# Kernel tuning notes

Measured on AMD Instinct MI355X. Metric: run time of the kernel, lower is better.

Reference implementation:

```python
import jax, jax.numpy as jnp
import numpy as np

B, S, D = 8, 1024, 1024
H = 2048            # expert hidden dim
E = 8               # num experts
TOP_K = 2
D_NOISE = 256
TEMP = 1.0


def setup_inputs() -> dict:
    key = jax.random.key(0)
    ks = jax.random.split(key, 8)
    return {
        "x": jax.random.normal(ks[0], (B, S, D), dtype=jnp.float32),
        "noise_clock_emb": jax.random.normal(ks[1], (B, D_NOISE), dtype=jnp.float32),
        # router weight [D_noise, E] (xavier-ish scale)
        "route_weight": jax.random.normal(ks[2], (D_NOISE, E), dtype=jnp.float32) * (1.0 / np.sqrt(D_NOISE)),
        # stacked expert params; torch Linear y = x @ W.T + b, stored here pre-transposed
        "fc_in_w": jax.random.normal(ks[3], (E, D, 2 * H), dtype=jnp.float32) * 0.02,
        "fc_in_b": jax.random.normal(ks[4], (E, 2 * H), dtype=jnp.float32) * 0.02,
        "fc_out_w": jax.random.normal(ks[5], (E, H, D), dtype=jnp.float32) * 0.02,
        "fc_out_b": jax.random.normal(ks[6], (E, D), dtype=jnp.float32) * 0.02,
    }


def reference(x, noise_clock_emb, route_weight, fc_in_w, fc_in_b, fc_out_w, fc_out_b):
    # ---- router: P = softmax(phi(sigma) @ W_R / T) ----
    logits = (noise_clock_emb @ route_weight) / TEMP            # [B, E]
    probs = jax.nn.softmax(logits, axis=-1)
    topk_weights, topk_indices = jax.lax.top_k(probs, TOP_K)    # [B, K]
    topk_weights = topk_weights / jnp.clip(
        topk_weights.sum(axis=-1, keepdims=True), 1e-8)
    # dense per-(batch, expert) mixing coefficient, identical to the
    # masked accumulation in the torch loop
    coeff = jnp.einsum("bke,bk->be",
                       jax.nn.one_hot(topk_indices, E, dtype=x.dtype),
                       topk_weights)                             # [B, E]

    # ---- all experts densely over the full batch (matches original math) ----
    h = jnp.einsum("bsd,edh->ebsh", x, fc_in_w) + fc_in_b[:, None, None, :]
    value, gate = jnp.split(h, 2, axis=-1)                       # [E,B,S,H] each
    hidden = value * jax.nn.silu(gate)
    mixed = jnp.einsum("ebsh,ehd,be->bsd", hidden, fc_out_w, coeff)
    mixed = mixed + jnp.einsum("be,ed->bd", coeff, fc_out_b)[:, None, :]
    return mixed, logits, probs, topk_indices, topk_weights
```

## Files before the change

### kernel.cpp

```cpp
#include <hip/hip_runtime.h>
#include <stdint.h>

#define B_ 8
#define S_ 1024
#define D_ 1024
#define H_ 2048
#define E_ 8
#define DN_ 256

typedef unsigned char u8;
typedef float f32x4 __attribute__((ext_vector_type(4)));
typedef long long ll;

__device__ __forceinline__ u8 f2f8(float f) {
  return (u8)(__builtin_amdgcn_cvt_pk_fp8_f32(f, f, 0, false) & 0xff);
}
__device__ __forceinline__ unsigned int pk4f8(float a, float b, float c, float d) {
  int w = __builtin_amdgcn_cvt_pk_fp8_f32(a, b, 0, false);
  w = __builtin_amdgcn_cvt_pk_fp8_f32(c, d, w, true);
  return (unsigned int)w;
}

__device__ __forceinline__ void gll16(const void* g, void* l) {
  __builtin_amdgcn_global_load_lds(
      (__attribute__((address_space(1))) void*)g,
      (__attribute__((address_space(3))) void*)l, 16, 0, 0);
}

__device__ __forceinline__ int swz(int r) { return (r & 3) ^ ((r >> 2) & 1); }

template <int R, int C>
__device__ __forceinline__ void transpose_body(const float* __restrict__ ip,
                                               u8* __restrict__ op,
                                               int bx, int by, int t,
                                               u8 (&tile)[64][72]) {
  const int r0 = by * 64, c0 = bx * 64;
  const int rr = t >> 4;
  const int c4 = t & 15;
#pragma unroll
  for (int i = 0; i < 4; ++i) {
    const int r = rr + i * 16;
    float4 v = *(const float4*)(ip + (size_t)(r0 + r) * C + c0 + c4 * 4);
    tile[c4 * 4 + 0][r] = f2f8(v.x);
    tile[c4 * 4 + 1][r] = f2f8(v.y);
    tile[c4 * 4 + 2][r] = f2f8(v.z);
    tile[c4 * 4 + 3][r] = f2f8(v.w);
  }
  __syncthreads();
#pragma unroll
  for (int i = 0; i < 4; ++i) {
    const int c = rr + i * 16;
    unsigned int w = *(const unsigned int*)&tile[c][c4 * 4];
    *(unsigned int*)(op + (size_t)(c0 + c) * R + r0 + c4 * 4) = w;
  }
}

#define NCAST (B_ * S_ * D_ / 1024)
#define NT1 ((2 * H_ / 64) * (D_ / 64) * E_)
#define NT2 ((D_ / 64) * (H_ / 64) * E_)

__global__ void __launch_bounds__(256) prep_kernel(
    const float* __restrict__ x, const float* __restrict__ noise,
    const float* __restrict__ rw, const float* __restrict__ fiw,
    const float* __restrict__ fow,
    float* __restrict__ out_logits, float* __restrict__ out_probs,
    float* __restrict__ out_idx, float* __restrict__ out_w,
    int* __restrict__ ws_idx, float* __restrict__ ws_w,
    unsigned int* __restrict__ xq, u8* __restrict__ wtin,
    u8* __restrict__ wtout) {
  __shared__ __align__(16) u8 tile[64][72];
  const int t = threadIdx.x;
  int bid = blockIdx.x;

  if (bid == 0) {
    float* sl = (float*)&tile[0][0];
    float* sp = sl + 64;
    {
      const int pair = t >> 2, sub = t & 3;
      const int b = pair >> 3, e = pair & 7;
      float acc = 0.f;
      const int d0 = sub * 64;
      for (int d = d0; d < d0 + 64; ++d)
        acc += noise[b * DN_ + d] * rw[d * E_ + e];
      acc += __shfl_xor(acc, 1);
      acc += __shfl_xor(acc, 2);
      if (sub == 0) sl[pair] = acc;
    }
    __syncthreads();
    if (t < 64) {
      const int b = t >> 3;
      float L = sl[t];
      out_logits[t] = L;
      float m = -1e30f;
      for (int j = 0; j < 8; ++j) m = fmaxf(m, sl[b * 8 + j]);
      float s = 0.f;
      for (int j = 0; j < 8; ++j) s += __expf(sl[b * 8 + j] - m);
      float p = __expf(L - m) / s;
      out_probs[t] = p;
      sp[t] = p;
    }
    __syncthreads();
    if (t < 64 && (t & 7) == 0) {
      const int b = t >> 3;
      int a1 = 0; float v1 = sp[b * 8];
      for (int j = 1; j < 8; ++j) { float v = sp[b * 8 + j]; if (v > v1) { v1 = v; a1 = j; } }
      int a2 = -1; float v2 = -1e30f;
      for (int j = 0; j < 8; ++j) {
        if (j == a1) continue;
        float v = sp[b * 8 + j]; if (v > v2) { v2 = v; a2 = j; }
      }
      float sum = fmaxf(v1 + v2, 1e-8f);
      float w1 = v1 / sum, w2 = v2 / sum;
      out_idx[b * 2] = (float)a1; out_idx[b * 2 + 1] = (float)a2;
      out_w[b * 2] = w1; out_w[b * 2 + 1] = w2;
      ws_idx[b * 2] = a1; ws_idx[b * 2 + 1] = a2;
      ws_w[b * 2] = w1; ws_w[b * 2 + 1] = w2;
    }
    return;
  }
  bid -= 1;
  if (bid < NCAST) {
    const size_t i = (size_t)bid * 256 + t;
    float4 v = *((const float4*)x + i);
    xq[i] = pk4f8(v.x, v.y, v.z, v.w);
    return;
  }
  bid -= NCAST;
  if (bid < NT1) {
    const int bx = bid & 63, by = (bid >> 6) & 15, e = bid >> 10;
    transpose_body<D_, 2 * H_>(fiw + (size_t)e * D_ * 2 * H_,
                               wtin + (size_t)e * D_ * 2 * H_, bx, by, t, tile);
    return;
  }
  bid -= NT1;
  {
    const int bx = bid & 15, by = (bid >> 4) & 31, e = bid >> 9;
    transpose_body<H_, D_>(fow + (size_t)e * H_ * D_,
                           wtout + (size_t)e * H_ * D_, bx, by, t, tile);
  }
}

__global__ void __launch_bounds__(256, 4) gemm1_kernel(
    const u8* __restrict__ xq,
    const u8* __restrict__ wtin,
    const float* __restrict__ bin,
    const int* __restrict__ ws_idx, const float* __restrict__ ws_w,
    u8* __restrict__ hid)
{
  const int nt = blockIdx.x;
  const int mt = blockIdx.y;
  const int z  = blockIdx.z;
  const int b  = z >> 1;
  const int e  = ws_idx[z] & 7;
  const float csc = ws_w[z];

  __shared__ u8 As[2][128 * 64];
  __shared__ u8 Bs[2][128 * 64];

  const int t = threadIdx.x;
  const int wave = t >> 6, lane = t & 63;
  const int wm = wave >> 1, wn = wave & 1;
  const int lm = lane & 15, lq = lane >> 4;
  const int lrow4 = lane >> 2;
  const int kq = ((lane & 3) ^ swz(lrow4)) * 16;
  const int fsw = swz(lm);
  const int p0 = lq >> 1, fb = (lq & 1) * 8;

  const u8* Ab  = xq + (size_t)b * (S_ * D_) + (size_t)mt * 128 * D_;
  const u8* Bvb = wtin + (size_t)e * (2 * H_ * D_) + (size_t)nt * 64 * D_;
  const u8* Bgb = Bvb + (size_t)H_ * D_;

  auto stage = [&](int bf, int kt) {
    const int k0 = kt * 64 + kq;
    gll16(Ab + (size_t)(wave * 16 + lrow4) * D_ + k0, (char*)As[bf] + wave * 1024);
    gll16(Ab + (size_t)((wave + 4) * 16 + lrow4) * D_ + k0, (char*)As[bf] + (wave + 4) * 1024);
    gll16(Bvb + (size_t)(wave * 16 + lrow4) * D_ + k0, (char*)Bs[bf] + wave * 1024);
    gll16(Bgb + (size_t)(wave * 16 + lrow4) * D_ + k0, (char*)Bs[bf] + 4096 + wave * 1024);
  };

  const f32x4 vz = {0.f, 0.f, 0.f, 0.f};
  f32x4 accv[4][2], accg[4][2];
#pragma unroll
  for (int i = 0; i < 4; ++i)
#pragma unroll
    for (int j = 0; j < 2; ++j) { accv[i][j] = vz; accg[i][j] = vz; }

  stage(0, 0);
  __syncthreads();
  int cur = 0;
#pragma unroll 2
  for (int kt = 0; kt < D_ / 64; ++kt) {
    if (kt + 1 < D_ / 64) stage(cur ^ 1, kt + 1);
    const u8* Asc = As[cur];
    const u8* Bsc = Bs[cur];
    ll af[4][2], bvf[2][2], bgf[2][2];
#pragma unroll
    for (int h = 0; h < 2; ++h) {
      const int pw = ((h * 2 + p0) ^ fsw) * 16 + fb;
#pragma unroll
      for (int i = 0; i < 4; ++i)
        af[i][h] = *(const ll*)(Asc + (wm * 64 + i * 16 + lm) * 64 + pw);
#pragma unroll
      for (int j = 0; j < 2; ++j) {
        bvf[j][h] = *(const ll*)(Bsc + (wn * 32 + j * 16 + lm) * 64 + pw);
        bgf[j][h] = *(const ll*)(Bsc + (64 + wn * 32 + j * 16 + lm) * 64 + pw);
      }
    }
#pragma unroll
    for (int h = 0; h < 2; ++h)
#pragma unroll
      for (int i = 0; i < 4; ++i)
#pragma unroll
        for (int j = 0; j < 2; ++j) {
          accv[i][j] = __builtin_amdgcn_mfma_f32_16x16x32_fp8_fp8(af[i][h], bvf[j][h], accv[i][j], 0, 0, 0);
          accg[i][j] = __builtin_amdgcn_mfma_f32_16x16x32_fp8_fp8(af[i][h], bgf[j][h], accg[i][j], 0, 0, 0);
        }
    __syncthreads();
    cur ^= 1;
  }

  u8* hb = hid + (size_t)z * (S_ * H_);
  const int row0 = mt * 128 + wm * 64;
  const int col0 = nt * 64 + wn * 32;
#pragma unroll
  for (int j = 0; j < 2; ++j) {
    const int col = col0 + j * 16 + lm;
    const float bvx = bin[e * 2 * H_ + col];
    const float bgx = bin[e * 2 * H_ + H_ + col];
#pragma unroll
    for (int i = 0; i < 4; ++i) {
#pragma unroll
      for (int r = 0; r < 4; ++r) {
        const int srow = row0 + i * 16 + lq * 4 + r;
        float v = accv[i][j][r] + bvx;
        float g = accg[i][j][r] + bgx;
        float hv = v * g / (1.f + __expf(-g)) * csc;
        hb[(size_t)srow * H_ + col] = f2f8(hv);
      }
    }
  }
}

__global__ void __launch_bounds__(256, 4) gemm2_kernel(
    const u8* __restrict__ hid,
    const u8* __restrict__ wtout,
    const float* __restrict__ bout,
    const int* __restrict__ ws_idx, const float* __restrict__ ws_w,
    float* __restrict__ out)
{
  const int nt = blockIdx.x;
  const int mt = blockIdx.y;
  const int b  = blockIdx.z;

  __shared__ u8 As[2][128 * 64];
  __shared__ u8 Bs[2][64 * 64];

  const int t = threadIdx.x;
  const int wave = t >> 6, lane = t & 63;
  const int wm = wave >> 1, wn = wave & 1;
  const int lm = lane & 15, lq = lane >> 4;
  const int lrow4 = lane >> 2;
  const int kq = ((lane & 3) ^ swz(lrow4)) * 16;
  const int fsw = swz(lm);
  const int p0 = lq >> 1, fb = (lq & 1) * 8;

  const int e0 = ws_idx[b * 2] & 7, e1 = ws_idx[b * 2 + 1] & 7;
  const u8* Ab0 = hid + ((size_t)(b * 2 + 0) * S_ + mt * 128) * H_;
  const u8* Ab1 = hid + ((size_t)(b * 2 + 1) * S_ + mt * 128) * H_;
  const u8* Bb0 = wtout + ((size_t)e0 * D_ + nt * 64) * H_;
  const u8* Bb1 = wtout + ((size_t)e1 * D_ + nt * 64) * H_;

  auto stage = [&](int bf, int it) {
    const u8* Ab = (it & 32) ? Ab1 : Ab0;
    const u8* Bb = (it & 32) ? Bb1 : Bb0;
    const int k0 = (it & 31) * 64 + kq;
    gll16(Ab + (size_t)(wave * 16 + lrow4) * H_ + k0, (char*)As[bf] + wave * 1024);
    gll16(Ab + (size_t)((wave + 4) * 16 + lrow4) * H_ + k0, (char*)As[bf] + (wave + 4) * 1024);
    gll16(Bb + (size_t)(wave * 16 + lrow4) * H_ + k0, (char*)Bs[bf] + wave * 1024);
  };

  const f32x4 vz = {0.f, 0.f, 0.f, 0.f};
  f32x4 acc[4][2];
#pragma unroll
  for (int i = 0; i < 4; ++i)
#pragma unroll
    for (int j = 0; j < 2; ++j) acc[i][j] = vz;

  stage(0, 0);
  __syncthreads();
  int cur = 0;
#pragma unroll 2
  for (int it = 0; it < 64; ++it) {
    if (it + 1 < 64) stage(cur ^ 1, it + 1);
    const u8* Asc = As[cur];
    const u8* Bsc = Bs[cur];
    ll af[4][2], bf[2][2];
#pragma unroll
    for (int h = 0; h < 2; ++h) {
      const int pw = ((h * 2 + p0) ^ fsw) * 16 + fb;
#pragma unroll
      for (int i = 0; i < 4; ++i)
        af[i][h] = *(const ll*)(Asc + (wm * 64 + i * 16 + lm) * 64 + pw);
#pragma unroll
      for (int j = 0; j < 2; ++j)
        bf[j][h] = *(const ll*)(Bsc + (wn * 32 + j * 16 + lm) * 64 + pw);
    }
#pragma unroll
    for (int h = 0; h < 2; ++h)
#pragma unroll
      for (int i = 0; i < 4; ++i)
#pragma unroll
        for (int j = 0; j < 2; ++j)
          acc[i][j] = __builtin_amdgcn_mfma_f32_16x16x32_fp8_fp8(af[i][h], bf[j][h], acc[i][j], 0, 0, 0);
    __syncthreads();
    cur ^= 1;
  }

  const float c0 = ws_w[b * 2], c1 = ws_w[b * 2 + 1];
  float* ob = out + (size_t)b * (S_ * D_);
  const int row0 = mt * 128 + wm * 64;
  const int col0 = nt * 64 + wn * 32;
#pragma unroll
  for (int j = 0; j < 2; ++j) {
    const int col = col0 + j * 16 + lm;
    const float bias = c0 * bout[e0 * D_ + col] + c1 * bout[e1 * D_ + col];
#pragma unroll
    for (int i = 0; i < 4; ++i)
#pragma unroll
      for (int r = 0; r < 4; ++r)
        ob[(size_t)(row0 + i * 16 + lq * 4 + r) * D_ + col] = acc[i][j][r] + bias;
  }
}

extern "C" void kernel_launch(void* const* d_in, const int* in_sizes, int n_in,
                              void* d_out, int out_size, void* d_ws, size_t ws_size,
                              hipStream_t stream) {
  const float* x     = (const float*)d_in[0];
  const float* noise = (const float*)d_in[1];
  const float* rw    = (const float*)d_in[2];
  const float* fiw   = (const float*)d_in[3];
  const float* fib   = (const float*)d_in[4];
  const float* fow   = (const float*)d_in[5];
  const float* fob   = (const float*)d_in[6];
  float* out = (float*)d_out;

  char* ws = (char*)d_ws;
  int*   ws_idx = (int*)ws;
  float* ws_w   = (float*)(ws + 64);
  u8* xq    = (u8*)(ws + 256);
  u8* wtin  = xq + (size_t)B_ * S_ * D_;
  u8* wtout = wtin + (size_t)E_ * 2 * H_ * D_;
  u8* hid   = wtout + (size_t)E_ * D_ * H_;

  float* out_mixed  = out;
  float* out_logits = out + (size_t)B_ * S_ * D_;
  float* out_probs  = out_logits + B_ * E_;
  float* out_idx    = out_probs + B_ * E_;
  float* out_w      = out_idx + B_ * 2;

  prep_kernel<<<1 + NCAST + NT1 + NT2, 256, 0, stream>>>(
      x, noise, rw, fiw, fow, out_logits, out_probs, out_idx, out_w,
      ws_idx, ws_w, (unsigned int*)xq, wtin, wtout);
  gemm1_kernel<<<dim3(32, 8, 16), 256, 0, stream>>>(xq, wtin, fib, ws_idx, ws_w, hid);
  gemm2_kernel<<<dim3(16, 8, 8), 256, 0, stream>>>(hid, wtout, fob, ws_idx, ws_w, out_mixed);
}
```

Measured before the change: 447.0 us.

## Pipeline GEMM k-loops with partial vmcnt waits and pack transpose writes

Both GEMM kernels replace the __syncthreads-based double buffer with explicit s_waitcnt vmcnt(N) plus raw s_barrier and sched_barrier fences. This lets the next stage's async global-to-LDS loads stay in flight while the current buffer is computed, with the last iterations peeled. The weight-transpose in the prep kernel now packs four fp8 values per u32 into a padded u32 tile and writes 16-byte vectors, replacing scattered byte stores. Launch bounds drop from 4 to 3 waves per SIMD to give the compiler more registers. The risk is that the hand-counted vmcnt values are wrong, which would let compute read LDS before the loads have landed.

```diff
diff --git a/kernel.cpp b/kernel.cpp
--- a/kernel.cpp
+++ b/kernel.cpp
@@ -9,16 +9,17 @@
 #define DN_ 256
 
 typedef unsigned char u8;
+typedef unsigned int u32;
 typedef float f32x4 __attribute__((ext_vector_type(4)));
 typedef long long ll;
 
 __device__ __forceinline__ u8 f2f8(float f) {
   return (u8)(__builtin_amdgcn_cvt_pk_fp8_f32(f, f, 0, false) & 0xff);
 }
-__device__ __forceinline__ unsigned int pk4f8(float a, float b, float c, float d) {
+__device__ __forceinline__ u32 pk4f8(float a, float b, float c, float d) {
   int w = __builtin_amdgcn_cvt_pk_fp8_f32(a, b, 0, false);
   w = __builtin_amdgcn_cvt_pk_fp8_f32(c, d, w, true);
-  return (unsigned int)w;
+  return (u32)w;
 }
 
 __device__ __forceinline__ void gll16(const void* g, void* l) {
@@ -33,26 +34,27 @@
 __device__ __forceinline__ void transpose_body(const float* __restrict__ ip,
                                                u8* __restrict__ op,
                                                int bx, int by, int t,
-                                               u8 (&tile)[64][72]) {
+                                               u32 (&tl)[64][17]) {
   const int r0 = by * 64, c0 = bx * 64;
-  const int rr = t >> 4;
-  const int c4 = t & 15;
-#pragma unroll
-  for (int i = 0; i < 4; ++i) {
-    const int r = rr + i * 16;
-    float4 v = *(const float4*)(ip + (size_t)(r0 + r) * C + c0 + c4 * 4);
-    tile[c4 * 4 + 0][r] = f2f8(v.x);
-    tile[c4 * 4 + 1][r] = f2f8(v.y);
-    tile[c4 * 4 + 2][r] = f2f8(v.z);
-    tile[c4 * 4 + 3][r] = f2f8(v.w);
-  }
+  const int rg = t >> 4;
+  const int cg = t & 15;
+  const float* p = ip + (size_t)(r0 + rg * 4) * C + c0 + cg * 4;
+  float4 v0 = *(const float4*)(p);
+  float4 v1 = *(const float4*)(p + C);
+  float4 v2 = *(const float4*)(p + 2 * C);
+  float4 v3 = *(const float4*)(p + 3 * C);
+  tl[cg * 4 + 0][rg] = pk4f8(v0.x, v1.x, v2.x, v3.x);
+  tl[cg * 4 + 1][rg] = pk4f8(v0.y, v1.y, v2.y, v3.y);
+  tl[cg * 4 + 2][rg] = pk4f8(v0.z, v1.z, v2.z, v3.z);
+  tl[cg * 4 + 3][rg] = pk4f8(v0.w, v1.w, v2.w, v3.w);
   __syncthreads();
-#pragma unroll
-  for (int i = 0; i < 4; ++i) {
-    const int c = rr + i * 16;
-    unsigned int w = *(const unsigned int*)&tile[c][c4 * 4];
-    *(unsigned int*)(op + (size_t)(c0 + c) * R + r0 + c4 * 4) = w;
-  }
+  const int c = t >> 2, q = t & 3;
+  uint4 w;
+  w.x = tl[c][q * 4 + 0];
+  w.y = tl[c][q * 4 + 1];
+  w.z = tl[c][q * 4 + 2];
+  w.w = tl[c][q * 4 + 3];
+  *(uint4*)(op + (size_t)(c0 + c) * R + r0 + q * 16) = w;
 }
 
 #define NCAST (B_ * S_ * D_ / 1024)
@@ -66,9 +68,9 @@
     float* __restrict__ out_logits, float* __restrict__ out_probs,
     float* __restrict__ out_idx, float* __restrict__ out_w,
     int* __restrict__ ws_idx, float* __restrict__ ws_w,
-    unsigned int* __restrict__ xq, u8* __restrict__ wtin,
+    u32* __restrict__ xq, u8* __restrict__ wtin,
     u8* __restrict__ wtout) {
-  __shared__ __align__(16) u8 tile[64][72];
+  __shared__ __align__(16) u32 tile[64][17];
   const int t = threadIdx.x;
   int bid = blockIdx.x;
 
@@ -140,7 +142,7 @@
   }
 }
 
-__global__ void __launch_bounds__(256, 4) gemm1_kernel(
+__global__ void __launch_bounds__(256, 3) gemm1_kernel(
     const u8* __restrict__ xq,
     const u8* __restrict__ wtin,
     const float* __restrict__ bin,
@@ -185,14 +187,9 @@
 #pragma unroll
     for (int j = 0; j < 2; ++j) { accv[i][j] = vz; accg[i][j] = vz; }
 
-  stage(0, 0);
-  __syncthreads();
-  int cur = 0;
-#pragma unroll 2
-  for (int kt = 0; kt < D_ / 64; ++kt) {
-    if (kt + 1 < D_ / 64) stage(cur ^ 1, kt + 1);
-    const u8* Asc = As[cur];
-    const u8* Bsc = Bs[cur];
+  auto compute = [&](int cb) {
+    const u8* Asc = As[cb];
+    const u8* Bsc = Bs[cb];
     ll af[4][2], bvf[2][2], bgf[2][2];
 #pragma unroll
     for (int h = 0; h < 2; ++h) {
@@ -215,9 +212,31 @@
           accv[i][j] = __builtin_amdgcn_mfma_f32_16x16x32_fp8_fp8(af[i][h], bvf[j][h], accv[i][j], 0, 0, 0);
           accg[i][j] = __builtin_amdgcn_mfma_f32_16x16x32_fp8_fp8(af[i][h], bgf[j][h], accg[i][j], 0, 0, 0);
         }
-    __syncthreads();
-    cur ^= 1;
-  }
+  };
+
+  stage(0, 0);
+#pragma unroll 2
+  for (int kt = 0; kt < 14; ++kt) {
+    const int cb = kt & 1;
+    stage(cb ^ 1, kt + 1);
+    asm volatile("s_waitcnt vmcnt(4)" ::: "memory");
+    __builtin_amdgcn_s_barrier();
+    __builtin_amdgcn_sched_barrier(0);
+    compute(cb);
+    __builtin_amdgcn_sched_barrier(0);
+    __builtin_amdgcn_s_barrier();
+  }
+  stage(1, 15);
+  asm volatile("s_waitcnt vmcnt(4)" ::: "memory");
+  __builtin_amdgcn_s_barrier();
+  __builtin_amdgcn_sched_barrier(0);
+  compute(0);
+  __builtin_amdgcn_sched_barrier(0);
+  __builtin_amdgcn_s_barrier();
+  asm volatile("s_waitcnt vmcnt(0)" ::: "memory");
+  __builtin_amdgcn_s_barrier();
+  __builtin_amdgcn_sched_barrier(0);
+  compute(1);
 
   u8* hb = hid + (size_t)z * (S_ * H_);
   const int row0 = mt * 128 + wm * 64;
@@ -241,7 +260,7 @@
   }
 }
 
-__global__ void __launch_bounds__(256, 4) gemm2_kernel(
+__global__ void __launch_bounds__(256, 3) gemm2_kernel(
     const u8* __restrict__ hid,
     const u8* __restrict__ wtout,
     const float* __restrict__ bout,
@@ -286,14 +305,9 @@
 #pragma unroll
     for (int j = 0; j < 2; ++j) acc[i][j] = vz;
 
-  stage(0, 0);
-  __syncthreads();
-  int cur = 0;
-#pragma unroll 2
-  for (int it = 0; it < 64; ++it) {
-    if (it + 1 < 64) stage(cur ^ 1, it + 1);
-    const u8* Asc = As[cur];
-    const u8* Bsc = Bs[cur];
+  auto compute = [&](int cb) {
+    const u8* Asc = As[cb];
+    const u8* Bsc = Bs[cb];
     ll af[4][2], bf[2][2];
 #pragma unroll
     for (int h = 0; h < 2; ++h) {
@@ -312,9 +326,31 @@
 #pragma unroll
         for (int j = 0; j < 2; ++j)
           acc[i][j] = __builtin_amdgcn_mfma_f32_16x16x32_fp8_fp8(af[i][h], bf[j][h], acc[i][j], 0, 0, 0);
-    __syncthreads();
-    cur ^= 1;
-  }
+  };
+
+  stage(0, 0);
+#pragma unroll 2
+  for (int it = 0; it < 62; ++it) {
+    const int cb = it & 1;
+    stage(cb ^ 1, it + 1);
+    asm volatile("s_waitcnt vmcnt(3)" ::: "memory");
+    __builtin_amdgcn_s_barrier();
+    __builtin_amdgcn_sched_barrier(0);
+    compute(cb);
+    __builtin_amdgcn_sched_barrier(0);
+    __builtin_amdgcn_s_barrier();
+  }
+  stage(1, 63);
+  asm volatile("s_waitcnt vmcnt(3)" ::: "memory");
+  __builtin_amdgcn_s_barrier();
+  __builtin_amdgcn_sched_barrier(0);
+  compute(0);
+  __builtin_amdgcn_sched_barrier(0);
+  __builtin_amdgcn_s_barrier();
+  asm volatile("s_waitcnt vmcnt(0)" ::: "memory");
+  __builtin_amdgcn_s_barrier();
+  __builtin_amdgcn_sched_barrier(0);
+  compute(1);
 
   const float c0 = ws_w[b * 2], c1 = ws_w[b * 2 + 1];
   float* ob = out + (size_t)b * (S_ * D_);
@@ -360,7 +396,7 @@
 
   prep_kernel<<<1 + NCAST + NT1 + NT2, 256, 0, stream>>>(
       x, noise, rw, fiw, fow, out_logits, out_probs, out_idx, out_w,
-      ws_idx, ws_w, (unsigned int*)xq, wtin, wtout);
+      ws_idx, ws_w, (u32*)xq, wtin, wtout);
   gemm1_kernel<<<dim3(32, 8, 16), 256, 0, stream>>>(xq, wtin, fib, ws_idx, ws_w, hid);
   gemm2_kernel<<<dim3(16, 8, 8), 256, 0, stream>>>(hid, wtout, fob, ws_idx, ws_w, out_mixed);
 }
```

Result: no change. 439.9 us (-1.6%).
